# Kernel optimization log

Measured on AMD Instinct MI355X. Metric: run time of the kernel, lower is better.

The kernel has to match this reference:

```python
import jax, jax.numpy as jnp
import numpy as np

BETA = 0.25


def setup_inputs() -> dict:
    key = jax.random.key(0)
    k1, k2 = jax.random.split(key)
    z = jax.random.normal(k1, (16, 1024, 256), dtype=jnp.float32)
    embedding = jax.random.normal(k2, (8192, 256), dtype=jnp.float32)
    return {"z": z, "embedding": embedding}


def reference(z, embedding):
    e_dim = embedding.shape[-1]
    z_flat = jnp.reshape(z, (-1, e_dim))  # [N, e_dim]
    # d[i,k] = ||z_i||^2 + ||e_k||^2 - 2 z_i . e_k  -> [N, n_e]
    d = (jnp.sum(z_flat ** 2, axis=1, keepdims=True)
         + jnp.sum(embedding ** 2, axis=1)
         - 2.0 * jnp.einsum('nd,kd->nk', z_flat, embedding))
    min_encoding_indices = jnp.argmin(d, axis=1)  # [N]
    z_q = embedding[min_encoding_indices]
    z_q = jnp.reshape(z_q, z.shape)
    loss = (jnp.mean((jax.lax.stop_gradient(z_q) - z) ** 2)
            + BETA * jnp.mean((z_q - jax.lax.stop_gradient(z)) ** 2))
    z_q = z + jax.lax.stop_gradient(z_q - z)  # straight-through estimator
    return (z_q, loss, min_encoding_indices)
```

## Files before the change

kernel.cpp:

```cpp
#include <hip/hip_runtime.h>
#include <stdint.h>

#define N_ROWS   16384
#define DIM      256
#define N_CODES  8192
#define ZQ_ELEMS 4194304

typedef _Float16 f16x8 __attribute__((ext_vector_type(8)));
typedef _Float16 f16x4 __attribute__((ext_vector_type(4)));
typedef float    f32x16 __attribute__((ext_vector_type(16)));
typedef unsigned long long u64;

#define WS_ET  0
#define WS_PK  (8650752)

static __device__ __forceinline__ void glds16(const void* gsrc, void* ldst) {
    __builtin_amdgcn_global_load_lds(
        (const __attribute__((address_space(1))) unsigned int*)gsrc,
        (__attribute__((address_space(3))) unsigned int*)ldst,
        16, 0, 0);
}

static __device__ __forceinline__ u64 packkey(float d, int c) {
    unsigned int u = __float_as_uint(d);
    u ^= ((unsigned int)((int)u >> 31)) | 0x80000000u;
    return ((u64)u << 32) | (unsigned int)c;
}

__global__ void vq_prep(const float* __restrict__ emb, const float* __restrict__ z,
                        _Float16* __restrict__ et, _Float16* __restrict__ zt,
                        float* __restrict__ loss_ptr) {
    __shared__ _Float16 shbuf[16896];
    const int t = threadIdx.x, w = t >> 6, l = t & 63;
    if (blockIdx.x < 2048) {
        if (blockIdx.x == 0 && t == 0) *loss_ptr = 0.0f;
        _Float16 (*lh)[264] = (_Float16(*)[264])shbuf;
        _Float16 (*ll)[264] = (_Float16(*)[264])(shbuf + 1056);
        const int code = blockIdx.x * 4 + w;
        float4 v = *(const float4*)(emb + (size_t)code * DIM + l * 4);
        float xs[4] = {v.x, v.y, v.z, v.w};
        f16x4 hh, lo;
        float s = 0.0f;
        #pragma unroll
        for (int i = 0; i < 4; ++i) {
            _Float16 h = (_Float16)xs[i];
            hh[i] = h;
            lo[i] = (_Float16)(xs[i] - (float)h);
            s += xs[i] * xs[i];
        }
        *(f16x4*)&lh[w][l * 4] = hh;
        *(f16x4*)&ll[w][l * 4] = lo;
        #pragma unroll
        for (int off = 32; off > 0; off >>= 1) s += __shfl_down(s, off, 64);
        if (l == 0) {
            _Float16 nh = (_Float16)s;
            _Float16 nl = (_Float16)(s - (float)nh);
            f16x8 aug, zr;
            #pragma unroll
            for (int i = 0; i < 8; ++i) { aug[i] = (_Float16)0; zr[i] = (_Float16)0; }
            aug[0] = nh; aug[1] = nl;
            *(f16x8*)(et + ((size_t)524288 + code) * 8) = aug;
            *(f16x8*)(et + ((size_t)532480 + code) * 8) = zr;
        }
        __syncthreads();
        const int p = t >> 7, g = t & 127;
        const int cl = g & 3, fg = g >> 2;
        f16x8 frag = (p == 0) ? *(const f16x8*)&lh[cl][fg * 8]
                              : *(const f16x8*)&ll[cl][fg * 8];
        const size_t unit = (size_t)p * 262144 + (size_t)(fg >> 1) * 16384
                          + (size_t)(blockIdx.x * 4 + cl) * 2 + (fg & 1);
        *(f16x8*)(et + unit * 8) = frag;
    } else {
        _Float16 (*ls)[32][264] = (_Float16(*)[32][264])shbuf;
        const int row0 = (blockIdx.x - 2048) * 32;
        #pragma unroll
        for (int j = 0; j < 8; ++j) {
            const int row = w * 8 + j;
            float4 v = *(const float4*)(z + (size_t)(row0 + row) * DIM + l * 4);
            float xs[4] = {v.x, v.y, v.z, v.w};
            f16x4 hh, lo;
            #pragma unroll
            for (int i = 0; i < 4; ++i) {
                const float m2 = -2.0f * xs[i];
                _Float16 h = (_Float16)m2;
                hh[i] = h;
                lo[i] = (_Float16)(m2 - (float)h);
            }
            *(f16x4*)&ls[0][row][l * 4] = hh;
            *(f16x4*)&ls[1][row][l * 4] = lo;
        }
        __syncthreads();
        #pragma unroll
        for (int pp = 0; pp < 8; ++pp) {
            const int gi = pp * 256 + t;
            const int p = gi >> 10, rem = gi & 1023;
            const int ksg = rem >> 6, rr = rem & 63;
            const int row = rr >> 1, h = rr & 1;
            f16x8 frag = *(const f16x8*)&ls[p][row][(2 * ksg + h) * 8];
            const size_t unit = (size_t)p * 524288 + (size_t)ksg * 32768
                              + (size_t)(row0 + row) * 2 + h;
            *(f16x8*)(zt + unit * 8) = frag;
        }
    }
}

__global__ __launch_bounds__(512, 2)
void vq_main(const _Float16* __restrict__ zt, const _Float16* __restrict__ et,
             u64* __restrict__ pkeys) {
    extern __shared__ char smem[];
    u64* run = (u64*)(smem + 131072);

    const int tid = threadIdx.x;
    const int w = tid >> 6, L = tid & 63, lo5 = L & 31, hi1 = L >> 5;
    const int rb = blockIdx.x >> 1, sp = blockIdx.x & 1;
    const int row0 = rb * 128, codeS = sp * 4096;

    #pragma unroll
    for (int i = 0; i < 16; ++i) {
        const int c = w * 16 + i;
        const int pl = c >> 6, cc = c & 63;
        glds16(zt + ((size_t)pl * 524288 + (size_t)(cc >> 2) * 32768
                     + (size_t)row0 * 2 + (cc & 3) * 64 + L) * 8,
               smem + ((c * 64 + L) << 4));
    }
    run[tid] = ~0ULL;
    run[tid + 512] = ~0ULL;
    __syncthreads();

    f16x8 bz;
    #pragma unroll
    for (int i = 0; i < 8; ++i) bz[i] = (_Float16)0;
    if (hi1 == 0) { bz[0] = (_Float16)1; bz[1] = (_Float16)1; }

    f32x16 zacc;
    #pragma unroll
    for (int e = 0; e < 16; ++e) zacc[e] = 0.0f;

    const f16x8* eb  = (const f16x8*)et;
    const f16x8* ebL = eb + 262144;
    const int laneU = lo5 * 2 + hi1;
    const char* zbH = smem + (lo5 * 32 + hi1 * 16);
    const char* zbL = zbH + 65536;

    f16x8 paug[2];
    {
        const int c0 = codeS + w * 64;
        paug[0] = eb[(size_t)(64 + hi1) * 8192 + c0 + lo5];
        paug[1] = eb[(size_t)(64 + hi1) * 8192 + c0 + 32 + lo5];
    }

    for (int ci = 0; ci < 8; ++ci) {
        const int c0 = codeS + ci * 512 + w * 64;
        f32x16 acc[2][4];

        __builtin_amdgcn_s_setprio(1);
        #pragma unroll
        for (int mt = 0; mt < 2; ++mt)
            #pragma unroll
            for (int nt = 0; nt < 4; ++nt)
                acc[mt][nt] = __builtin_amdgcn_mfma_f32_32x32x16_f16(paug[mt], bz, zacc, 0, 0, 0);
        __builtin_amdgcn_s_setprio(0);

        if (ci < 7) {
            const int c1 = codeS + (ci + 1) * 512 + w * 64;
            paug[0] = eb[(size_t)(64 + hi1) * 8192 + c1 + lo5];
            paug[1] = eb[(size_t)(64 + hi1) * 8192 + c1 + 32 + lo5];
        }

        const size_t cu = (size_t)c0 * 2 + laneU;
        #pragma unroll 4
        for (int ksg = 0; ksg < 16; ++ksg) {
            const size_t ub = (size_t)ksg * 16384 + cu;
            f16x8 ah[2], al[2];
            ah[0] = eb[ub];       ah[1] = eb[ub + 64];
            al[0] = ebL[ub];      al[1] = ebL[ub + 64];
            f16x8 bh[4], bl[4];
            #pragma unroll
            for (int nt = 0; nt < 4; ++nt) {
                bh[nt] = *(const f16x8*)(zbH + (ksg * 4096 + nt * 1024));
                bl[nt] = *(const f16x8*)(zbL + (ksg * 4096 + nt * 1024));
            }
            __builtin_amdgcn_s_setprio(1);
            #pragma unroll
            for (int mt = 0; mt < 2; ++mt)
                #pragma unroll
                for (int nt = 0; nt < 4; ++nt) {
                    acc[mt][nt] = __builtin_amdgcn_mfma_f32_32x32x16_f16(ah[mt], bh[nt], acc[mt][nt], 0, 0, 0);
                    acc[mt][nt] = __builtin_amdgcn_mfma_f32_32x32x16_f16(ah[mt], bl[nt], acc[mt][nt], 0, 0, 0);
                    acc[mt][nt] = __builtin_amdgcn_mfma_f32_32x32x16_f16(al[mt], bh[nt], acc[mt][nt], 0, 0, 0);
                }
            __builtin_amdgcn_s_setprio(0);
        }

        #pragma unroll
        for (int nt = 0; nt < 4; ++nt) {
            float mm[16];
            #pragma unroll
            for (int r = 0; r < 16; ++r)
                mm[r] = fminf(acc[0][nt][r], acc[1][nt][r]);
            #pragma unroll
            for (int s2 = 8; s2 > 0; s2 >>= 1)
                #pragma unroll
                for (int r = 0; r < 8; ++r)
                    if (r < s2) mm[r] = fminf(mm[r], mm[r + s2]);
            const float m = mm[0];
            int rel = 64;
            #pragma unroll
            for (int mt = 0; mt < 2; ++mt)
                #pragma unroll
                for (int r = 0; r < 16; ++r) {
                    const int rc = mt * 32 + (r & 3) + 8 * (r >> 2);
                    const int cand = (acc[mt][nt][r] == m) ? rc : 64;
                    rel = cand < rel ? cand : rel;
                }
            u64 best = packkey(m, c0 + 4 * hi1 + rel);
            const u64 o = __shfl_xor(best, 32, 64);
            if (o < best) best = o;
            if (hi1 == 0) {
                u64* p = &run[w * 128 + nt * 32 + lo5];
                if (best < *p) *p = best;
            }
        }
    }

    __syncthreads();
    if (tid < 128) {
        u64 k = run[tid];
        #pragma unroll
        for (int w2 = 1; w2 < 8; ++w2) { u64 o = run[w2 * 128 + tid]; if (o < k) k = o; }
        pkeys[(size_t)sp * N_ROWS + row0 + tid] = k;
    }
}

__global__ __launch_bounds__(512)
void vq_final(const float* __restrict__ z, const float* __restrict__ emb,
              const u64* __restrict__ pkeys,
              float* __restrict__ zq_out, float* __restrict__ loss_out,
              float* __restrict__ idx_out) {
    __shared__ int best[64];
    const int t = threadIdx.x;
    const int row0 = blockIdx.x * 64;
    if (t < 64) {
        u64 k = pkeys[row0 + t];
        u64 o = pkeys[(size_t)N_ROWS + row0 + t];
        if (o < k) k = o;
        const int code = (int)(k & 0xFFFFFFFFu);
        best[t] = code;
        idx_out[row0 + t] = (float)code;
    }
    __syncthreads();
    const int wave = t >> 6, lane = t & 63;
    float lsum = 0.0f;
    #pragma unroll
    for (int rr = 0; rr < 8; ++rr) {
        const int rl = wave * 8 + rr;
        const int rg = row0 + rl;
        const int code = best[rl];
        float4 ev = *(const float4*)(emb + (size_t)code * DIM + lane * 4);
        float4 zv = *(const float4*)(z   + (size_t)rg   * DIM + lane * 4);
        float dx = ev.x - zv.x, dy = ev.y - zv.y;
        float dz = ev.z - zv.z, dw = ev.w - zv.w;
        lsum += dx * dx + dy * dy + dz * dz + dw * dw;
        *(float4*)(zq_out + (size_t)rg * DIM + lane * 4) = ev;
    }
    #pragma unroll
    for (int off = 32; off > 0; off >>= 1) lsum += __shfl_down(lsum, off, 64);
    if (lane == 0) atomicAdd(loss_out, lsum * (1.25f / (float)ZQ_ELEMS));
}

extern "C" void kernel_launch(void* const* d_in, const int* in_sizes, int n_in,
                              void* d_out, int out_size, void* d_ws, size_t ws_size,
                              hipStream_t stream) {
    const float* z   = (const float*)d_in[0];
    const float* emb = (const float*)d_in[1];
    float* out  = (float*)d_out;
    float* zq   = out;
    float* loss = out + ZQ_ELEMS;
    float* idx  = out + ZQ_ELEMS + 1;

    char* ws = (char*)d_ws;
    _Float16* et = (_Float16*)(ws + WS_ET);
    u64*   pk    = (u64*)(ws + WS_PK);

    _Float16* zt = (_Float16*)zq;

    static bool attr_set = false;
    if (!attr_set) {
        hipFuncSetAttribute((const void*)vq_main,
                            hipFuncAttributeMaxDynamicSharedMemorySize, 139264);
        attr_set = true;
    }

    vq_prep<<<2560, 256, 0, stream>>>(emb, z, et, zt, loss);
    vq_main<<<256, 512, 139264, stream>>>(zt, et, pk);
    vq_final<<<N_ROWS / 64, 512, 0, stream>>>(z, emb, pk, zq, loss, idx);
}
```

Baseline: 278.9 us.

## Fuse z split-conversion into main kernel and halve row tile for occupancy

The main kernel now reads fp32 z directly and converts it to hi/lo fp16 pairs in padded LDS, removing the z transposition pass from the prep kernel and its scratch buffer. The row tile per block drops from 128 to 64, which halves LDS use and doubles the grid to 512 blocks, with launch bounds raised to allow more resident blocks per CU. The prep kernel is restructured to handle 32 codes per block and no longer writes the zero augment row. The trade-off is that each codebook fragment loaded from global memory now feeds half as many row tiles, roughly doubling global/L2 traffic for the codebook.

```diff
diff --git a/kernel.cpp b/kernel.cpp
--- a/kernel.cpp
+++ b/kernel.cpp
@@ -14,30 +14,22 @@
 #define WS_ET  0
 #define WS_PK  (8650752)
 
-static __device__ __forceinline__ void glds16(const void* gsrc, void* ldst) {
-    __builtin_amdgcn_global_load_lds(
-        (const __attribute__((address_space(1))) unsigned int*)gsrc,
-        (__attribute__((address_space(3))) unsigned int*)ldst,
-        16, 0, 0);
-}
-
 static __device__ __forceinline__ u64 packkey(float d, int c) {
     unsigned int u = __float_as_uint(d);
     u ^= ((unsigned int)((int)u >> 31)) | 0x80000000u;
     return ((u64)u << 32) | (unsigned int)c;
 }
 
-__global__ void vq_prep(const float* __restrict__ emb, const float* __restrict__ z,
-                        _Float16* __restrict__ et, _Float16* __restrict__ zt,
+__global__ void vq_prep(const float* __restrict__ emb, _Float16* __restrict__ et,
                         float* __restrict__ loss_ptr) {
-    __shared__ _Float16 shbuf[16896];
+    __shared__ _Float16 sh[2][32][272];
     const int t = threadIdx.x, w = t >> 6, l = t & 63;
-    if (blockIdx.x < 2048) {
-        if (blockIdx.x == 0 && t == 0) *loss_ptr = 0.0f;
-        _Float16 (*lh)[264] = (_Float16(*)[264])shbuf;
-        _Float16 (*ll)[264] = (_Float16(*)[264])(shbuf + 1056);
-        const int code = blockIdx.x * 4 + w;
-        float4 v = *(const float4*)(emb + (size_t)code * DIM + l * 4);
+    if (blockIdx.x == 0 && t == 0) *loss_ptr = 0.0f;
+    const int code0 = blockIdx.x * 32;
+    #pragma unroll
+    for (int j = 0; j < 8; ++j) {
+        const int cl = w * 8 + j;
+        float4 v = *(const float4*)(emb + (size_t)(code0 + cl) * DIM + l * 4);
         float xs[4] = {v.x, v.y, v.z, v.w};
         f16x4 hh, lo;
         float s = 0.0f;
@@ -48,84 +40,63 @@
             lo[i] = (_Float16)(xs[i] - (float)h);
             s += xs[i] * xs[i];
         }
-        *(f16x4*)&lh[w][l * 4] = hh;
-        *(f16x4*)&ll[w][l * 4] = lo;
+        *(f16x4*)&sh[0][cl][l * 4] = hh;
+        *(f16x4*)&sh[1][cl][l * 4] = lo;
         #pragma unroll
         for (int off = 32; off > 0; off >>= 1) s += __shfl_down(s, off, 64);
         if (l == 0) {
             _Float16 nh = (_Float16)s;
             _Float16 nl = (_Float16)(s - (float)nh);
-            f16x8 aug, zr;
-            #pragma unroll
-            for (int i = 0; i < 8; ++i) { aug[i] = (_Float16)0; zr[i] = (_Float16)0; }
+            f16x8 aug;
+            #pragma unroll
+            for (int i = 0; i < 8; ++i) aug[i] = (_Float16)0;
             aug[0] = nh; aug[1] = nl;
-            *(f16x8*)(et + ((size_t)524288 + code) * 8) = aug;
-            *(f16x8*)(et + ((size_t)532480 + code) * 8) = zr;
-        }
-        __syncthreads();
-        const int p = t >> 7, g = t & 127;
-        const int cl = g & 3, fg = g >> 2;
-        f16x8 frag = (p == 0) ? *(const f16x8*)&lh[cl][fg * 8]
-                              : *(const f16x8*)&ll[cl][fg * 8];
-        const size_t unit = (size_t)p * 262144 + (size_t)(fg >> 1) * 16384
-                          + (size_t)(blockIdx.x * 4 + cl) * 2 + (fg & 1);
+            *(f16x8*)(et + ((size_t)524288 + code0 + cl) * 8) = aug;
+        }
+    }
+    __syncthreads();
+    #pragma unroll
+    for (int pp = 0; pp < 8; ++pp) {
+        const int gi = pp * 256 + t;
+        const int p = gi >> 10, ks = (gi >> 6) & 15, cl = (gi >> 1) & 31, h = gi & 1;
+        f16x8 frag = *(const f16x8*)&sh[p][cl][ks * 16 + h * 8];
+        const size_t unit = (size_t)p * 262144 + (size_t)ks * 16384
+                          + (size_t)(code0 + cl) * 2 + h;
         *(f16x8*)(et + unit * 8) = frag;
-    } else {
-        _Float16 (*ls)[32][264] = (_Float16(*)[32][264])shbuf;
-        const int row0 = (blockIdx.x - 2048) * 32;
-        #pragma unroll
-        for (int j = 0; j < 8; ++j) {
-            const int row = w * 8 + j;
-            float4 v = *(const float4*)(z + (size_t)(row0 + row) * DIM + l * 4);
-            float xs[4] = {v.x, v.y, v.z, v.w};
-            f16x4 hh, lo;
-            #pragma unroll
-            for (int i = 0; i < 4; ++i) {
-                const float m2 = -2.0f * xs[i];
-                _Float16 h = (_Float16)m2;
-                hh[i] = h;
-                lo[i] = (_Float16)(m2 - (float)h);
-            }
-            *(f16x4*)&ls[0][row][l * 4] = hh;
-            *(f16x4*)&ls[1][row][l * 4] = lo;
-        }
-        __syncthreads();
-        #pragma unroll
-        for (int pp = 0; pp < 8; ++pp) {
-            const int gi = pp * 256 + t;
-            const int p = gi >> 10, rem = gi & 1023;
-            const int ksg = rem >> 6, rr = rem & 63;
-            const int row = rr >> 1, h = rr & 1;
-            f16x8 frag = *(const f16x8*)&ls[p][row][(2 * ksg + h) * 8];
-            const size_t unit = (size_t)p * 524288 + (size_t)ksg * 32768
-                              + (size_t)(row0 + row) * 2 + h;
-            *(f16x8*)(zt + unit * 8) = frag;
-        }
-    }
-}
-
-__global__ __launch_bounds__(512, 2)
-void vq_main(const _Float16* __restrict__ zt, const _Float16* __restrict__ et,
+    }
+}
+
+__global__ __launch_bounds__(512, 4)
+void vq_main(const float* __restrict__ z, const _Float16* __restrict__ et,
              u64* __restrict__ pkeys) {
     extern __shared__ char smem[];
-    u64* run = (u64*)(smem + 131072);
+    u64* run = (u64*)(smem + 66560);
 
     const int tid = threadIdx.x;
     const int w = tid >> 6, L = tid & 63, lo5 = L & 31, hi1 = L >> 5;
     const int rb = blockIdx.x >> 1, sp = blockIdx.x & 1;
-    const int row0 = rb * 128, codeS = sp * 4096;
-
-    #pragma unroll
-    for (int i = 0; i < 16; ++i) {
-        const int c = w * 16 + i;
-        const int pl = c >> 6, cc = c & 63;
-        glds16(zt + ((size_t)pl * 524288 + (size_t)(cc >> 2) * 32768
-                     + (size_t)row0 * 2 + (cc & 3) * 64 + L) * 8,
-               smem + ((c * 64 + L) << 4));
+    const int row0 = rb * 64, codeS = sp * 4096;
+
+    const float* zr = z + (size_t)row0 * DIM;
+    #pragma unroll
+    for (int jj = 0; jj < 8; ++jj) {
+        const int idx = jj * 512 + tid;
+        const int r = idx >> 6, q = idx & 63;
+        float4 v = *(const float4*)(zr + (size_t)r * DIM + q * 4);
+        float xs[4] = {v.x, v.y, v.z, v.w};
+        f16x4 hh, lo;
+        #pragma unroll
+        for (int i = 0; i < 4; ++i) {
+            const float m2 = -2.0f * xs[i];
+            _Float16 h = (_Float16)m2;
+            hh[i] = h;
+            lo[i] = (_Float16)(m2 - (float)h);
+        }
+        char* base = smem + r * 1040 + q * 8;
+        *(f16x4*)(base) = hh;
+        *(f16x4*)(base + 512) = lo;
     }
     run[tid] = ~0ULL;
-    run[tid + 512] = ~0ULL;
-    __syncthreads();
 
     f16x8 bz;
     #pragma unroll
@@ -139,32 +110,32 @@
     const f16x8* eb  = (const f16x8*)et;
     const f16x8* ebL = eb + 262144;
     const int laneU = lo5 * 2 + hi1;
-    const char* zbH = smem + (lo5 * 32 + hi1 * 16);
-    const char* zbL = zbH + 65536;
+    const char* zb = smem + (lo5 * 1040 + hi1 * 16);
 
     f16x8 paug[2];
     {
         const int c0 = codeS + w * 64;
-        paug[0] = eb[(size_t)(64 + hi1) * 8192 + c0 + lo5];
-        paug[1] = eb[(size_t)(64 + hi1) * 8192 + c0 + 32 + lo5];
-    }
+        paug[0] = eb[(size_t)524288 + c0 + lo5];
+        paug[1] = eb[(size_t)524288 + c0 + 32 + lo5];
+    }
+    __syncthreads();
 
     for (int ci = 0; ci < 8; ++ci) {
         const int c0 = codeS + ci * 512 + w * 64;
-        f32x16 acc[2][4];
+        f32x16 acc[2][2];
 
         __builtin_amdgcn_s_setprio(1);
         #pragma unroll
         for (int mt = 0; mt < 2; ++mt)
             #pragma unroll
-            for (int nt = 0; nt < 4; ++nt)
+            for (int nt = 0; nt < 2; ++nt)
                 acc[mt][nt] = __builtin_amdgcn_mfma_f32_32x32x16_f16(paug[mt], bz, zacc, 0, 0, 0);
         __builtin_amdgcn_s_setprio(0);
 
         if (ci < 7) {
             const int c1 = codeS + (ci + 1) * 512 + w * 64;
-            paug[0] = eb[(size_t)(64 + hi1) * 8192 + c1 + lo5];
-            paug[1] = eb[(size_t)(64 + hi1) * 8192 + c1 + 32 + lo5];
+            paug[0] = eb[(size_t)524288 + c1 + lo5];
+            paug[1] = eb[(size_t)524288 + c1 + 32 + lo5];
         }
 
         const size_t cu = (size_t)c0 * 2 + laneU;
@@ -174,17 +145,17 @@
             f16x8 ah[2], al[2];
             ah[0] = eb[ub];       ah[1] = eb[ub + 64];
             al[0] = ebL[ub];      al[1] = ebL[ub + 64];
-            f16x8 bh[4], bl[4];
-            #pragma unroll
-            for (int nt = 0; nt < 4; ++nt) {
-                bh[nt] = *(const f16x8*)(zbH + (ksg * 4096 + nt * 1024));
-                bl[nt] = *(const f16x8*)(zbL + (ksg * 4096 + nt * 1024));
+            f16x8 bh[2], bl[2];
+            #pragma unroll
+            for (int nt = 0; nt < 2; ++nt) {
+                bh[nt] = *(const f16x8*)(zb + (ksg * 32 + nt * 33280));
+                bl[nt] = *(const f16x8*)(zb + (ksg * 32 + nt * 33280 + 512));
             }
             __builtin_amdgcn_s_setprio(1);
             #pragma unroll
             for (int mt = 0; mt < 2; ++mt)
                 #pragma unroll
-                for (int nt = 0; nt < 4; ++nt) {
+                for (int nt = 0; nt < 2; ++nt) {
                     acc[mt][nt] = __builtin_amdgcn_mfma_f32_32x32x16_f16(ah[mt], bh[nt], acc[mt][nt], 0, 0, 0);
                     acc[mt][nt] = __builtin_amdgcn_mfma_f32_32x32x16_f16(ah[mt], bl[nt], acc[mt][nt], 0, 0, 0);
                     acc[mt][nt] = __builtin_amdgcn_mfma_f32_32x32x16_f16(al[mt], bh[nt], acc[mt][nt], 0, 0, 0);
@@ -193,7 +164,7 @@
         }
 
         #pragma unroll
-        for (int nt = 0; nt < 4; ++nt) {
+        for (int nt = 0; nt < 2; ++nt) {
             float mm[16];
             #pragma unroll
             for (int r = 0; r < 16; ++r)
@@ -217,17 +188,17 @@
             const u64 o = __shfl_xor(best, 32, 64);
             if (o < best) best = o;
             if (hi1 == 0) {
-                u64* p = &run[w * 128 + nt * 32 + lo5];
+                u64* p = &run[w * 64 + nt * 32 + lo5];
                 if (best < *p) *p = best;
             }
         }
     }
 
     __syncthreads();
-    if (tid < 128) {
+    if (tid < 64) {
         u64 k = run[tid];
         #pragma unroll
-        for (int w2 = 1; w2 < 8; ++w2) { u64 o = run[w2 * 128 + tid]; if (o < k) k = o; }
+        for (int w2 = 1; w2 < 8; ++w2) { u64 o = run[w2 * 64 + tid]; if (o < k) k = o; }
         pkeys[(size_t)sp * N_ROWS + row0 + tid] = k;
     }
 }
@@ -282,16 +253,14 @@
     _Float16* et = (_Float16*)(ws + WS_ET);
     u64*   pk    = (u64*)(ws + WS_PK);
 
-    _Float16* zt = (_Float16*)zq;
-
     static bool attr_set = false;
     if (!attr_set) {
         hipFuncSetAttribute((const void*)vq_main,
-                            hipFuncAttributeMaxDynamicSharedMemorySize, 139264);
+                            hipFuncAttributeMaxDynamicSharedMemorySize, 70656);
         attr_set = true;
     }
 
-    vq_prep<<<2560, 256, 0, stream>>>(emb, z, et, zt, loss);
-    vq_main<<<256, 512, 139264, stream>>>(zt, et, pk);
+    vq_prep<<<256, 256, 0, stream>>>(emb, et, loss);
+    vq_main<<<512, 512, 70656, stream>>>(z, et, pk);
     vq_final<<<N_ROWS / 64, 512, 0, stream>>>(z, emb, pk, zq, loss, idx);
 }
```

Result: slower. 294.7 us (+5.7%).
